# Kernel tuning notes

Hardware: AMD Instinct MI355X
Metric: run time of the kernel (lower is better)

## Reference

```python
import jax, jax.numpy as jnp
import numpy as np

N_SEGMENTS = 50000  # number of destination nodes (index values in [0, N_SEGMENTS))


def setup_inputs() -> dict:
    key = jax.random.key(0)
    k1, k2 = jax.random.split(key)
    input = jax.random.normal(k1, (1600000, 64), dtype=jnp.float32)
    index = jax.random.randint(k2, (1600000,), 0, N_SEGMENTS, dtype=jnp.int64)
    return {"input": input, "index": index}


def reference(input, index):
    # Sum-aggregate rows of `input` grouped by `index`: out[n] = sum_{e: index[e]==n} input[e]
    # Equivalent to the custom loma_sum_aggr forward (scatter-add segmented reduction).
    return jax.ops.segment_sum(input, index, num_segments=N_SEGMENTS)
```

## Files before the change

### kernel.cpp

```cpp
#include <hip/hip_runtime.h>

#define N_SEGMENTS 50000
#define N_ROWS     1600000
#define N_FEAT     64

__global__ void seg_sum_atomic(const float* __restrict__ in,
                               const int*   __restrict__ idx,
                               float*       __restrict__ out) {
    long long t   = (long long)blockIdx.x * blockDim.x + threadIdx.x;
    long long row = t >> 6;
    int       c   = (int)(t & 63);
    if (row < (long long)N_ROWS) {
        int s = idx[row];
        float v = in[row * N_FEAT + c];
        atomicAdd(out + (long long)s * N_FEAT + c, v);
    }
}

__global__ void hist_kernel(const int* __restrict__ idx, int* __restrict__ cnt) {
    int t = blockIdx.x * blockDim.x + threadIdx.x;
    int r = t << 2;
    if (r < N_ROWS) {
        int4 v = *reinterpret_cast<const int4*>(idx + r);
        atomicAdd(&cnt[v.x], 1);
        atomicAdd(&cnt[v.y], 1);
        atomicAdd(&cnt[v.z], 1);
        atomicAdd(&cnt[v.w], 1);
    }
}

__global__ void __launch_bounds__(1024) scan_kernel(const int* __restrict__ cnt,
                                                    int* __restrict__ base,
                                                    int* __restrict__ cursor) {
    __shared__ int part[1024];
    int t = threadIdx.x;
    const int CHUNK = (N_SEGMENTS + 1023) / 1024;
    int lo = t * CHUNK;
    int hi = lo + CHUNK; if (hi > N_SEGMENTS) hi = N_SEGMENTS;
    if (lo > N_SEGMENTS) lo = N_SEGMENTS;
    int sum = 0;
    for (int i = lo; i < hi; ++i) sum += cnt[i];
    part[t] = sum;
    __syncthreads();
    for (int ofs = 1; ofs < 1024; ofs <<= 1) {
        int v = (t >= ofs) ? part[t - ofs] : 0;
        __syncthreads();
        part[t] += v;
        __syncthreads();
    }
    int run = (t == 0) ? 0 : part[t - 1];
    for (int i = lo; i < hi; ++i) {
        base[i]   = run;
        cursor[i] = run;
        run += cnt[i];
    }
    if (t == 1023) base[N_SEGMENTS] = N_ROWS;
}

__global__ void scatter_kernel(const int* __restrict__ idx,
                               int* __restrict__ cursor,
                               int* __restrict__ rowids) {
    int t = blockIdx.x * blockDim.x + threadIdx.x;
    int r = t << 2;
    if (r < N_ROWS) {
        int4 v = *reinterpret_cast<const int4*>(idx + r);
        rowids[atomicAdd(&cursor[v.x], 1)] = r;
        rowids[atomicAdd(&cursor[v.y], 1)] = r + 1;
        rowids[atomicAdd(&cursor[v.z], 1)] = r + 2;
        rowids[atomicAdd(&cursor[v.w], 1)] = r + 3;
    }
}

__device__ __forceinline__ float4 fadd4(float4 a, float4 b) {
    a.x += b.x; a.y += b.y; a.z += b.z; a.w += b.w; return a;
}

__global__ void gather_kernel(const float* __restrict__ in,
                              const int*   __restrict__ rowids,
                              const int*   __restrict__ base,
                              float*       __restrict__ out) {
    int wave = (blockIdx.x * blockDim.x + threadIdx.x) >> 6;
    int lane = threadIdx.x & 63;
    if (wave >= N_SEGMENTS) return;
    int q = lane >> 4;
    int f = lane & 15;
    int beg = base[wave];
    int end = base[wave + 1];
    float4 z = {0.f, 0.f, 0.f, 0.f};
    float4 a0 = z, a1 = z, a2 = z, a3 = z;

    for (int j0 = beg; j0 < end; j0 += 64) {
        int n = end - j0; if (n > 64) n = 64;
        int myid = (lane < n) ? rowids[j0 + lane] : 0;
        for (int k = 0; k < n; k += 16) {
            int i0 = k + q, i1 = k + 4 + q, i2 = k + 8 + q, i3 = k + 12 + q;
            int r0 = __shfl(myid, i0 < n ? i0 : 0);
            int r1 = __shfl(myid, i1 < n ? i1 : 0);
            int r2 = __shfl(myid, i2 < n ? i2 : 0);
            int r3 = __shfl(myid, i3 < n ? i3 : 0);
            float4 v0 = *reinterpret_cast<const float4*>(in + (long long)r0 * N_FEAT + f * 4);
            float4 v1 = *reinterpret_cast<const float4*>(in + (long long)r1 * N_FEAT + f * 4);
            float4 v2 = *reinterpret_cast<const float4*>(in + (long long)r2 * N_FEAT + f * 4);
            float4 v3 = *reinterpret_cast<const float4*>(in + (long long)r3 * N_FEAT + f * 4);
            if (i0 < n) a0 = fadd4(a0, v0);
            if (i1 < n) a1 = fadd4(a1, v1);
            if (i2 < n) a2 = fadd4(a2, v2);
            if (i3 < n) a3 = fadd4(a3, v3);
        }
    }

    float4 a = fadd4(fadd4(a0, a1), fadd4(a2, a3));
    a.x += __shfl_xor(a.x, 16); a.y += __shfl_xor(a.y, 16);
    a.z += __shfl_xor(a.z, 16); a.w += __shfl_xor(a.w, 16);
    a.x += __shfl_xor(a.x, 32); a.y += __shfl_xor(a.y, 32);
    a.z += __shfl_xor(a.z, 32); a.w += __shfl_xor(a.w, 32);

    if (q == 0) {
        *reinterpret_cast<float4*>(out + (size_t)wave * N_FEAT + f * 4) = a;
    }
}

extern "C" void kernel_launch(void* const* d_in, const int* in_sizes, int n_in,
                              void* d_out, int out_size, void* d_ws, size_t ws_size,
                              hipStream_t stream) {
    const float* in  = (const float*)d_in[0];
    const int*   idx = (const int*)d_in[1];
    float*       out = (float*)d_out;

    const size_t need = ((size_t)N_SEGMENTS * 3 + 1 + N_ROWS) * sizeof(int);
    if (ws_size < need) {
        hipMemsetAsync(d_out, 0, (size_t)out_size * sizeof(float), stream);
        const long long total = (long long)N_ROWS * N_FEAT;
        const int block = 256;
        const long long grid = (total + block - 1) / block;
        seg_sum_atomic<<<(unsigned)grid, block, 0, stream>>>(in, idx, out);
        return;
    }

    int* cnt    = (int*)d_ws;
    int* base   = cnt + N_SEGMENTS;
    int* cursor = base + N_SEGMENTS + 1;
    int* rowids = cursor + N_SEGMENTS;

    hipMemsetAsync(cnt, 0, (size_t)N_SEGMENTS * sizeof(int), stream);

    const int block = 256;
    const int gridRows = (N_ROWS / 4 + block - 1) / block;
    hist_kernel   <<<gridRows, block, 0, stream>>>(idx, cnt);
    scan_kernel   <<<1, 1024, 0, stream>>>(cnt, base, cursor);
    scatter_kernel<<<gridRows, block, 0, stream>>>(idx, cursor, rowids);

    const int gridGather = (N_SEGMENTS * 64) / 256;
    gather_kernel <<<gridGather, block, 0, stream>>>(in, rowids, base, out);
}
```

Measured before the change: 838.6 us.

## Parallelize offset scan across blocks and use nontemporal unrolled gather loads

Replaces the single-block serial-chunk prefix scan over segment counts with a multi-block scan: each block scans a contiguous chunk, and a small fix-up kernel scans the chunk totals into per-chunk offsets. Scatter and gather add those offsets on the fly. The gather loop is now fully unrolled to a fixed 64-iteration body, and it uses nontemporal vector loads and stores to cut cache pollution from the streamed input. This adds one extra kernel launch and an offset lookup on every scatter and gather access.

```diff
diff --git a/kernel.cpp b/kernel.cpp
--- a/kernel.cpp
+++ b/kernel.cpp
@@ -3,6 +3,10 @@
 #define N_SEGMENTS 50000
 #define N_ROWS     1600000
 #define N_FEAT     64
+#define SCHUNK     1000
+#define N_CHUNKS   50
+
+typedef float f32x4 __attribute__((ext_vector_type(4)));
 
 __global__ void seg_sum_atomic(const float* __restrict__ in,
                                const int*   __restrict__ idx,
@@ -29,79 +33,91 @@
     }
 }
 
-__global__ void __launch_bounds__(1024) scan_kernel(const int* __restrict__ cnt,
-                                                    int* __restrict__ base,
-                                                    int* __restrict__ cursor) {
+__global__ void __launch_bounds__(1024) scan_part(const int* __restrict__ cnt,
+                                                  int* __restrict__ base,
+                                                  int* __restrict__ cursor,
+                                                  int* __restrict__ csum) {
     __shared__ int part[1024];
+    int b = blockIdx.x;
     int t = threadIdx.x;
-    const int CHUNK = (N_SEGMENTS + 1023) / 1024;
-    int lo = t * CHUNK;
-    int hi = lo + CHUNK; if (hi > N_SEGMENTS) hi = N_SEGMENTS;
-    if (lo > N_SEGMENTS) lo = N_SEGMENTS;
-    int sum = 0;
-    for (int i = lo; i < hi; ++i) sum += cnt[i];
-    part[t] = sum;
+    int g = b * SCHUNK + t;
+    part[t] = (t < SCHUNK) ? cnt[g] : 0;
     __syncthreads();
     for (int ofs = 1; ofs < 1024; ofs <<= 1) {
-        int v = (t >= ofs) ? part[t - ofs] : 0;
+        int u = (t >= ofs) ? part[t - ofs] : 0;
         __syncthreads();
-        part[t] += v;
+        part[t] += u;
         __syncthreads();
     }
-    int run = (t == 0) ? 0 : part[t - 1];
-    for (int i = lo; i < hi; ++i) {
-        base[i]   = run;
-        cursor[i] = run;
-        run += cnt[i];
+    int excl = (t == 0) ? 0 : part[t - 1];
+    if (t < SCHUNK) { base[g] = excl; cursor[g] = excl; }
+    if (t == 1023) csum[b] = part[1023];
+}
+
+__global__ void scan_fix(const int* __restrict__ csum,
+                         int* __restrict__ off,
+                         int* __restrict__ base) {
+    int t = threadIdx.x;
+    int orig = (t < N_CHUNKS) ? csum[t] : 0;
+    int v = orig;
+    for (int ofs = 1; ofs < 64; ofs <<= 1) {
+        int u = __shfl_up(v, ofs);
+        if (t >= ofs) v += u;
     }
-    if (t == 1023) base[N_SEGMENTS] = N_ROWS;
+    if (t < N_CHUNKS) off[t] = v - orig;
+    if (t == N_CHUNKS - 1) { off[N_CHUNKS] = v; base[N_SEGMENTS] = 0; }
 }
 
 __global__ void scatter_kernel(const int* __restrict__ idx,
                                int* __restrict__ cursor,
+                               const int* __restrict__ off,
                                int* __restrict__ rowids) {
     int t = blockIdx.x * blockDim.x + threadIdx.x;
     int r = t << 2;
     if (r < N_ROWS) {
         int4 v = *reinterpret_cast<const int4*>(idx + r);
-        rowids[atomicAdd(&cursor[v.x], 1)] = r;
-        rowids[atomicAdd(&cursor[v.y], 1)] = r + 1;
-        rowids[atomicAdd(&cursor[v.z], 1)] = r + 2;
-        rowids[atomicAdd(&cursor[v.w], 1)] = r + 3;
+        rowids[atomicAdd(&cursor[v.x], 1) + off[v.x / SCHUNK]] = r;
+        rowids[atomicAdd(&cursor[v.y], 1) + off[v.y / SCHUNK]] = r + 1;
+        rowids[atomicAdd(&cursor[v.z], 1) + off[v.z / SCHUNK]] = r + 2;
+        rowids[atomicAdd(&cursor[v.w], 1) + off[v.w / SCHUNK]] = r + 3;
     }
 }
 
-__device__ __forceinline__ float4 fadd4(float4 a, float4 b) {
-    a.x += b.x; a.y += b.y; a.z += b.z; a.w += b.w; return a;
-}
+__device__ __forceinline__ f32x4 fadd4(f32x4 a, f32x4 b) { return a + b; }
 
 __global__ void gather_kernel(const float* __restrict__ in,
                               const int*   __restrict__ rowids,
                               const int*   __restrict__ base,
+                              const int*   __restrict__ off,
                               float*       __restrict__ out) {
     int wave = (blockIdx.x * blockDim.x + threadIdx.x) >> 6;
     int lane = threadIdx.x & 63;
     if (wave >= N_SEGMENTS) return;
     int q = lane >> 4;
     int f = lane & 15;
-    int beg = base[wave];
-    int end = base[wave + 1];
-    float4 z = {0.f, 0.f, 0.f, 0.f};
-    float4 a0 = z, a1 = z, a2 = z, a3 = z;
+    int beg = base[wave]     + off[wave / SCHUNK];
+    int end = base[wave + 1] + off[(wave + 1) / SCHUNK];
+    f32x4 z = {0.f, 0.f, 0.f, 0.f};
+    f32x4 a0 = z, a1 = z, a2 = z, a3 = z;
 
     for (int j0 = beg; j0 < end; j0 += 64) {
         int n = end - j0; if (n > 64) n = 64;
         int myid = (lane < n) ? rowids[j0 + lane] : 0;
-        for (int k = 0; k < n; k += 16) {
+#pragma unroll
+        for (int k = 0; k < 64; k += 16) {
             int i0 = k + q, i1 = k + 4 + q, i2 = k + 8 + q, i3 = k + 12 + q;
             int r0 = __shfl(myid, i0 < n ? i0 : 0);
             int r1 = __shfl(myid, i1 < n ? i1 : 0);
             int r2 = __shfl(myid, i2 < n ? i2 : 0);
             int r3 = __shfl(myid, i3 < n ? i3 : 0);
-            float4 v0 = *reinterpret_cast<const float4*>(in + (long long)r0 * N_FEAT + f * 4);
-            float4 v1 = *reinterpret_cast<const float4*>(in + (long long)r1 * N_FEAT + f * 4);
-            float4 v2 = *reinterpret_cast<const float4*>(in + (long long)r2 * N_FEAT + f * 4);
-            float4 v3 = *reinterpret_cast<const float4*>(in + (long long)r3 * N_FEAT + f * 4);
+            f32x4 v0 = __builtin_nontemporal_load(
+                reinterpret_cast<const f32x4*>(in + (long long)r0 * N_FEAT + f * 4));
+            f32x4 v1 = __builtin_nontemporal_load(
+                reinterpret_cast<const f32x4*>(in + (long long)r1 * N_FEAT + f * 4));
+            f32x4 v2 = __builtin_nontemporal_load(
+                reinterpret_cast<const f32x4*>(in + (long long)r2 * N_FEAT + f * 4));
+            f32x4 v3 = __builtin_nontemporal_load(
+                reinterpret_cast<const f32x4*>(in + (long long)r3 * N_FEAT + f * 4));
             if (i0 < n) a0 = fadd4(a0, v0);
             if (i1 < n) a1 = fadd4(a1, v1);
             if (i2 < n) a2 = fadd4(a2, v2);
@@ -109,14 +125,15 @@
         }
     }
 
-    float4 a = fadd4(fadd4(a0, a1), fadd4(a2, a3));
+    f32x4 a = fadd4(fadd4(a0, a1), fadd4(a2, a3));
     a.x += __shfl_xor(a.x, 16); a.y += __shfl_xor(a.y, 16);
     a.z += __shfl_xor(a.z, 16); a.w += __shfl_xor(a.w, 16);
     a.x += __shfl_xor(a.x, 32); a.y += __shfl_xor(a.y, 32);
     a.z += __shfl_xor(a.z, 32); a.w += __shfl_xor(a.w, 32);
 
     if (q == 0) {
-        *reinterpret_cast<float4*>(out + (size_t)wave * N_FEAT + f * 4) = a;
+        __builtin_nontemporal_store(a,
+            reinterpret_cast<f32x4*>(out + (size_t)wave * N_FEAT + f * 4));
     }
 }
 
@@ -127,9 +144,9 @@
     const int*   idx = (const int*)d_in[1];
     float*       out = (float*)d_out;
 
-    const size_t need = ((size_t)N_SEGMENTS * 3 + 1 + N_ROWS) * sizeof(int);
+    const size_t need = ((size_t)N_SEGMENTS * 3 + 1 + 128 + N_ROWS) * sizeof(int);
     if (ws_size < need) {
-        hipMemsetAsync(d_out, 0, (size_t)out_size * sizeof(float), stream);
+        (void)hipMemsetAsync(d_out, 0, (size_t)out_size * sizeof(float), stream);
         const long long total = (long long)N_ROWS * N_FEAT;
         const int block = 256;
         const long long grid = (total + block - 1) / block;
@@ -140,16 +157,19 @@
     int* cnt    = (int*)d_ws;
     int* base   = cnt + N_SEGMENTS;
     int* cursor = base + N_SEGMENTS + 1;
-    int* rowids = cursor + N_SEGMENTS;
+    int* csum   = cursor + N_SEGMENTS;
+    int* off    = csum + 64;
+    int* rowids = off + 64;
 
-    hipMemsetAsync(cnt, 0, (size_t)N_SEGMENTS * sizeof(int), stream);
+    (void)hipMemsetAsync(cnt, 0, (size_t)N_SEGMENTS * sizeof(int), stream);
 
     const int block = 256;
     const int gridRows = (N_ROWS / 4 + block - 1) / block;
     hist_kernel   <<<gridRows, block, 0, stream>>>(idx, cnt);
-    scan_kernel   <<<1, 1024, 0, stream>>>(cnt, base, cursor);
-    scatter_kernel<<<gridRows, block, 0, stream>>>(idx, cursor, rowids);
+    scan_part     <<<N_CHUNKS, 1024, 0, stream>>>(cnt, base, cursor, csum);
+    scan_fix      <<<1, 64, 0, stream>>>(csum, off, base);
+    scatter_kernel<<<gridRows, block, 0, stream>>>(idx, cursor, off, rowids);
 
     const int gridGather = (N_SEGMENTS * 64) / 256;
-    gather_kernel <<<gridGather, block, 0, stream>>>(in, rowids, base, out);
+    gather_kernel <<<gridGather, block, 0, stream>>>(in, rowids, base, off, out);
 }
```

Result: faster. 705.5 us (-15.9%).
